# Kernel tuning notes

Hardware: AMD Instinct MI355X
Metric: run time of the kernel (lower is better)

## Reference

```python
import jax, jax.numpy as jnp
import numpy as np

B, H, W, C = 8, 64, 64, 256
RC = C // 8  # reduced channels per build()

def setup_inputs() -> dict:
    key = jax.random.key(0)
    ks = jax.random.split(key, 4)
    x = jax.random.normal(ks[0], (B, H, W, C), dtype=jnp.float32)
    # 1x1 conv kernels flattened to [Cin, Cout]; glorot-ish scale
    wq = jax.random.normal(ks[1], (C, RC), dtype=jnp.float32) * (1.0 / np.sqrt(C))
    wk = jax.random.normal(ks[2], (C, RC), dtype=jnp.float32) * (1.0 / np.sqrt(C))
    wv = jax.random.normal(ks[3], (C, C), dtype=jnp.float32) * (1.0 / np.sqrt(C))
    bq = jnp.zeros((RC,), dtype=jnp.float32)
    bk = jnp.zeros((RC,), dtype=jnp.float32)
    bv = jnp.zeros((C,), dtype=jnp.float32)
    return {"x": x, "wq": wq, "bq": bq, "wk": wk, "bk": bk, "wv": wv, "bv": bv}

def reference(x, wq, bq, wk, bk, wv, bv):
    b, h, w, c = x.shape
    n = h * w
    # 1x1 convs == per-pixel channel matmuls; q/k have relu activation, v does not
    q = jax.nn.relu(jnp.einsum('bhwc,cd->bhwd', x, wq) + bq).reshape(b, n, -1)  # [B,N,RC]
    k = jax.nn.relu(jnp.einsum('bhwc,cd->bhwd', x, wk) + bk).reshape(b, n, -1)  # [B,N,RC]
    v = (jnp.einsum('bhwc,cd->bhwd', x, wv) + bv).reshape(b, n, c)              # [B,N,C]
    attn = jax.nn.softmax(jnp.einsum('bnd,bmd->bnm', q, k), axis=-1)            # [B,N,N]
    out = jnp.einsum('bnm,bmc->bnc', attn, v).reshape(b, h, w, c)
    return out + x
```

## Files before the change

kernel.cpp:

```cpp
#include <hip/hip_runtime.h>
#include <hip/hip_bf16.h>

typedef __attribute__((ext_vector_type(8))) short s16x8;
typedef __attribute__((ext_vector_type(4))) float f32x4;
typedef __attribute__((ext_vector_type(4))) unsigned int u32x4;

#define BATCH 8
#define NPIX  4096
#define CCH   256
#define RCH   32
#define TK    32
#define HALFK 2048
#define NIT   (HALFK / TK)
#define THR   8.0f
#define LOG2E 1.4426950408889634f

__device__ __forceinline__ unsigned short f2bf(float f) {
  __hip_bfloat16 h = __float2bfloat16(f);
  return __builtin_bit_cast(unsigned short, h);
}

__device__ __forceinline__ unsigned int cvt_pk(float lo, float hi) {
  unsigned int r;
  asm("v_cvt_pk_bf16_f32 %0, %1, %2" : "=v"(r) : "v"(lo), "v"(hi));
  return r;
}

__global__ void prep_kernel(const float* __restrict__ x,
                            const float* __restrict__ wq,
                            const float* __restrict__ wk,
                            const float* __restrict__ wv,
                            unsigned short* __restrict__ xb,
                            unsigned short* __restrict__ wqkT,
                            unsigned short* __restrict__ wvT) {
  int stride = gridDim.x * blockDim.x;
  int i0 = blockIdx.x * blockDim.x + threadIdx.x;
  const int nx4 = BATCH * NPIX * CCH / 4;
  for (int i = i0; i < nx4; i += stride) {
    float4 v = reinterpret_cast<const float4*>(x)[i];
    ushort4 o;
    o.x = f2bf(v.x); o.y = f2bf(v.y); o.z = f2bf(v.z); o.w = f2bf(v.w);
    reinterpret_cast<ushort4*>(xb)[i] = o;
  }
  for (int i = i0; i < 64 * CCH; i += stride) {
    int d = i >> 8, c = i & 255;
    float v = (d < RCH) ? wq[c * RCH + d] : wk[c * RCH + (d - RCH)];
    wqkT[i] = f2bf(v);
  }
  for (int i = i0; i < CCH * CCH; i += stride) {
    int d = i >> 8, c = i & 255;
    wvT[i] = f2bf(wv[c * CCH + d]);
  }
}

__global__ void proj_kernel(const unsigned short* __restrict__ xb,
                            const unsigned short* __restrict__ wqkT,
                            const unsigned short* __restrict__ wvT,
                            const float* __restrict__ bq,
                            const float* __restrict__ bk,
                            const float* __restrict__ bv,
                            unsigned short* __restrict__ qb,
                            unsigned short* __restrict__ kb,
                            unsigned short* __restrict__ vT) {
  int t = threadIdx.x;
  int w = t >> 6, l = t & 63, g = l >> 4, lc = l & 15;
  f32x4 zero = {0.f, 0.f, 0.f, 0.f};

  if (blockIdx.x < 512) {
    int row0 = blockIdx.x * 64 + w * 16;
    f32x4 acc[4];
    for (int ct = 0; ct < 4; ++ct) acc[ct] = zero;
    for (int ks = 0; ks < 8; ++ks) {
      s16x8 a = *reinterpret_cast<const s16x8*>(
          xb + (size_t)(row0 + lc) * CCH + ks * 32 + g * 8);
      for (int ct = 0; ct < 4; ++ct) {
        s16x8 bfr = *reinterpret_cast<const s16x8*>(
            wqkT + (size_t)(ct * 16 + lc) * CCH + ks * 32 + g * 8);
        acc[ct] = __builtin_amdgcn_mfma_f32_16x16x32_bf16(a, bfr, acc[ct], 0, 0, 0);
      }
    }
    for (int ct = 0; ct < 4; ++ct) {
      int col = ct * 16 + lc;
      float bias = (col < RCH) ? bq[col] : bk[col - RCH];
      for (int r = 0; r < 4; ++r) {
        int row = row0 + 4 * g + r;
        float v = fmaxf(acc[ct][r] + bias, 0.f);
        if (col < RCH) qb[(size_t)row * RCH + col] = f2bf(v * LOG2E);
        else           kb[(size_t)row * RCH + (col - RCH)] = f2bf(v);
      }
    }
  } else {
    int idx = blockIdx.x - 512;
    int b = idx & 7; idx >>= 3;
    int dt = idx & 3; int nt = idx >> 2;
    int d0 = dt * 64 + w * 16;
    int n0 = nt * 64;
    f32x4 acc[4];
    for (int ct = 0; ct < 4; ++ct) acc[ct] = zero;
    for (int ks = 0; ks < 8; ++ks) {
      s16x8 a = *reinterpret_cast<const s16x8*>(
          wvT + (size_t)(d0 + lc) * CCH + ks * 32 + g * 8);
      for (int ct = 0; ct < 4; ++ct) {
        s16x8 bfr = *reinterpret_cast<const s16x8*>(
            xb + ((size_t)b * NPIX + n0 + ct * 16 + lc) * CCH + ks * 32 + g * 8);
        acc[ct] = __builtin_amdgcn_mfma_f32_16x16x32_bf16(a, bfr, acc[ct], 0, 0, 0);
      }
    }
    for (int ct = 0; ct < 4; ++ct) {
      for (int r = 0; r < 4; ++r) {
        int d = d0 + 4 * g + r;
        int n = n0 + ct * 16 + lc;
        vT[((size_t)b * CCH + d) * NPIX + n] = f2bf(acc[ct][r] + bv[d]);
      }
    }
  }
}

__global__ __launch_bounds__(256, 2)
void attn_kernel(const unsigned short* __restrict__ qb,
                 const unsigned short* __restrict__ kb,
                 const unsigned short* __restrict__ vT,
                 const float* __restrict__ x,
                 float* __restrict__ out) {
  __shared__ __attribute__((aligned(16))) unsigned short Vlds[2][CCH * 64];
  __shared__ __attribute__((aligned(16))) float mergeLS[2][32];
  __shared__ float mLds[2];

  int b  = blockIdx.x & 7;
  int qt = blockIdx.x >> 3;
  int t  = threadIdx.x;
  int w = t >> 6, l = t & 63, g = l >> 4, lc = l & 15;
  int a = w >> 1, s = w & 1;
  const size_t bN = (size_t)b * NPIX;
  f32x4 zero = {0.f, 0.f, 0.f, 0.f};

  const unsigned short* kbase = kb + bN * RCH;
  const unsigned short* vbase = vT + (size_t)b * CCH * NPIX;

  int qbase = qt * 64 + a * 32;
  s16x8 qfA = *reinterpret_cast<const s16x8*>(qb + (bN + qbase + lc) * RCH + g * 8);
  s16x8 qfB = *reinterpret_cast<const s16x8*>(qb + (bN + qbase + 16 + lc) * RCH + g * 8);

  int chb = t >> 3, gr = t & 7;
  int gsw = gr ^ (chb & 7);
  int koff = (gsw < 4) ? (gsw * 8) : (HALFK + (gsw - 4) * 8);
  const unsigned short* vsrc = vbase + (size_t)chb * NPIX + koff;

  int krb = 8 * (lc >> 2) + (lc & 3);
  int kO  = s * HALFK + krb;

  unsigned int swz = (lc & 7) << 4;
  int vrS = (s * 64 + g * 16) ^ swz;

  s16x8 ones;
  #pragma unroll
  for (int i = 0; i < 8; ++i) ones[i] = (short)0x3F80;

  f32x4 o[2][16];
  #pragma unroll
  for (int qh = 0; qh < 2; ++qh)
    #pragma unroll
    for (int cc = 0; cc < 16; ++cc) o[qh][cc] = zero;
  f32x4 ols[2];
  ols[0] = zero; ols[1] = zero;
  float m = 0.f;
  f32x4 mneg = zero;

  s16x8 gv[8];
  #pragma unroll
  for (int i = 0; i < 8; ++i)
    gv[i] = *reinterpret_cast<const s16x8*>(vsrc + (size_t)i * 32 * NPIX);
  s16x8 kf0 = *reinterpret_cast<const s16x8*>(kbase + (size_t)(kO + 0) * RCH + g * 8);
  s16x8 kf1 = *reinterpret_cast<const s16x8*>(kbase + (size_t)(kO + 4) * RCH + g * 8);
  #pragma unroll
  for (int i = 0; i < 8; ++i)
    *reinterpret_cast<s16x8*>((char*)&Vlds[0][0] + i * 4096 + t * 16) = gv[i];

  for (int it = 0; it < NIT; ++it) {
    int p = it & 1;
    int kv = it * TK;
    bool nx = (it + 1) < NIT;

    if (nx) {
      #pragma unroll
      for (int i = 0; i < 8; ++i)
        gv[i] = *reinterpret_cast<const s16x8*>(
            vsrc + kv + TK + (size_t)i * 32 * NPIX);
    }

    f32x4 sA0 = __builtin_amdgcn_mfma_f32_16x16x32_bf16(kf0, qfA, mneg, 0, 0, 0);
    f32x4 sA1 = __builtin_amdgcn_mfma_f32_16x16x32_bf16(kf1, qfA, mneg, 0, 0, 0);
    f32x4 sB0 = __builtin_amdgcn_mfma_f32_16x16x32_bf16(kf0, qfB, mneg, 0, 0, 0);
    f32x4 sB1 = __builtin_amdgcn_mfma_f32_16x16x32_bf16(kf1, qfB, mneg, 0, 0, 0);

    if (nx) {
      kf0 = *reinterpret_cast<const s16x8*>(
          kbase + (size_t)(kO + kv + TK + 0) * RCH + g * 8);
      kf1 = *reinterpret_cast<const s16x8*>(
          kbase + (size_t)(kO + kv + TK + 4) * RCH + g * 8);
    }

    float xA = fmaxf(fmaxf(sA0[0], sA0[1]), fmaxf(sA0[2], sA0[3]));
    float xB = fmaxf(fmaxf(sA1[0], sA1[1]), fmaxf(sA1[2], sA1[3]));
    float xC = fmaxf(fmaxf(sB0[0], sB0[1]), fmaxf(sB0[2], sB0[3]));
    float xD = fmaxf(fmaxf(sB1[0], sB1[1]), fmaxf(sB1[2], sB1[3]));
    float pmax = fmaxf(fmaxf(xA, xB), fmaxf(xC, xD));

    float sc = 1.f;
    int resc = !__all(pmax <= THR);
    if (resc) {
      #pragma unroll
      for (int off = 1; off <= 32; off <<= 1)
        pmax = fmaxf(pmax, __shfl_xor(pmax, off));
      float delta = fmaxf(pmax, 0.f);
      sc = exp2f(-delta);
      m += delta;
      f32x4 dd = {delta, delta, delta, delta};
      mneg -= dd;
      sA0 -= dd; sA1 -= dd; sB0 -= dd; sB1 -= dd;
      #pragma unroll
      for (int qh = 0; qh < 2; ++qh) {
        #pragma unroll
        for (int cc = 0; cc < 16; ++cc)
          #pragma unroll
          for (int r = 0; r < 4; ++r) o[qh][cc][r] *= sc;
        #pragma unroll
        for (int r = 0; r < 4; ++r) ols[qh][r] *= sc;
      }
    }

    unsigned int pkA[4], pkB[4];
    pkA[0] = cvt_pk(exp2f(sA0[0]), exp2f(sA0[1]));
    pkA[1] = cvt_pk(exp2f(sA0[2]), exp2f(sA0[3]));
    pkA[2] = cvt_pk(exp2f(sA1[0]), exp2f(sA1[1]));
    pkA[3] = cvt_pk(exp2f(sA1[2]), exp2f(sA1[3]));
    pkB[0] = cvt_pk(exp2f(sB0[0]), exp2f(sB0[1]));
    pkB[1] = cvt_pk(exp2f(sB0[2]), exp2f(sB0[3]));
    pkB[2] = cvt_pk(exp2f(sB1[0]), exp2f(sB1[1]));
    pkB[3] = cvt_pk(exp2f(sB1[2]), exp2f(sB1[3]));

    u32x4 uA = {pkA[0], pkA[1], pkA[2], pkA[3]};
    u32x4 uB = {pkB[0], pkB[1], pkB[2], pkB[3]};
    s16x8 paA = __builtin_bit_cast(s16x8, uA);
    s16x8 paB = __builtin_bit_cast(s16x8, uB);
    ols[0] = __builtin_amdgcn_mfma_f32_16x16x32_bf16(paA, ones, ols[0], 0, 0, 0);
    ols[1] = __builtin_amdgcn_mfma_f32_16x16x32_bf16(paB, ones, ols[1], 0, 0, 0);

    asm volatile("s_waitcnt lgkmcnt(0)" ::: "memory");
    __builtin_amdgcn_s_barrier();
    asm volatile("" ::: "memory");

    const char* pb = (const char*)&Vlds[p][0] + lc * 128 + vrS;
    __builtin_amdgcn_s_setprio(1);
    #pragma unroll
    for (int cc = 0; cc < 16; ++cc) {
      s16x8 vb = *reinterpret_cast<const s16x8*>(pb + cc * 2048);
      o[0][cc] = __builtin_amdgcn_mfma_f32_16x16x32_bf16(paA, vb, o[0][cc], 0, 0, 0);
      o[1][cc] = __builtin_amdgcn_mfma_f32_16x16x32_bf16(paB, vb, o[1][cc], 0, 0, 0);
    }
    __builtin_amdgcn_s_setprio(0);

    if (nx) {
      #pragma unroll
      for (int i = 0; i < 8; ++i)
        *reinterpret_cast<s16x8*>((char*)&Vlds[p ^ 1][0] + i * 4096 + t * 16) = gv[i];
    }
  }

  if (s == 1) {
    if (lc == 0) {
      *reinterpret_cast<f32x4*>(&mergeLS[a][4 * g])      = ols[0];
      *reinterpret_cast<f32x4*>(&mergeLS[a][16 + 4 * g]) = ols[1];
    }
    if (l == 0) mLds[a] = m;
  }
  __syncthreads();

  float* mrg = (float*)&Vlds[0][0];
  if (s == 1) {
    float* base = mrg + a * 8192 + l * 128;
    #pragma unroll
    for (int qh = 0; qh < 2; ++qh)
      #pragma unroll
      for (int cc = 0; cc < 16; ++cc) {
        int idx = qh * 16 + cc;
        *reinterpret_cast<f32x4*>(base + ((idx + l) & 31) * 4) = o[qh][cc];
      }
  }
  __syncthreads();
  if (s == 0) {
    float mB = mLds[a];
    float mT = fmaxf(m, mB);
    float sAc = exp2f(m - mT), sBc = exp2f(mB - mT);
    const float* base = mrg + a * 8192 + l * 128;
    #pragma unroll
    for (int qh = 0; qh < 2; ++qh) {
      f32x4 lB4 = *reinterpret_cast<const f32x4*>(&mergeLS[a][qh * 16 + 4 * g]);
      f32x4 rl;
      #pragma unroll
      for (int r = 0; r < 4; ++r)
        rl[r] = 1.0f / (ols[qh][r] * sAc + lB4[r] * sBc);
      #pragma unroll
      for (int cc = 0; cc < 16; ++cc) {
        int idx = qh * 16 + cc;
        f32x4 ob = *reinterpret_cast<const f32x4*>(base + ((idx + l) & 31) * 4);
        #pragma unroll
        for (int r = 0; r < 4; ++r) {
          size_t row = bN + qbase + qh * 16 + 4 * g + r;
          size_t oi = row * CCH + cc * 16 + lc;
          out[oi] = (o[qh][cc][r] * sAc + ob[r] * sBc) * rl[r] + x[oi];
        }
      }
    }
  }
}

extern "C" void kernel_launch(void* const* d_in, const int* in_sizes, int n_in,
                              void* d_out, int out_size, void* d_ws, size_t ws_size,
                              hipStream_t stream) {
  const float* x  = (const float*)d_in[0];
  const float* wq = (const float*)d_in[1];
  const float* bq = (const float*)d_in[2];
  const float* wk = (const float*)d_in[3];
  const float* bk = (const float*)d_in[4];
  const float* wv = (const float*)d_in[5];
  const float* bv = (const float*)d_in[6];
  float* out = (float*)d_out;

  unsigned short* ws   = (unsigned short*)d_ws;
  unsigned short* qb   = ws;
  unsigned short* kb   = qb + 1048576;
  unsigned short* vT   = kb + 1048576;
  unsigned short* xb   = vT + 8388608;
  unsigned short* wqkT = xb + 8388608;
  unsigned short* wvT  = wqkT + 16384;

  prep_kernel<<<dim3(2048), dim3(256), 0, stream>>>(x, wq, wk, wv, xb, wqkT, wvT);
  proj_kernel<<<dim3(2560), dim3(256), 0, stream>>>(xb, wqkT, wvT, bq, bk, bv,
                                                    qb, kb, vT);
  attn_kernel<<<dim3(512), dim3(256), 0, stream>>>(qb, kb, vT, x, out);
}
```

Baseline: 166.6 us.

## Software-pipeline QK softmax one tile ahead and stream V via direct global-to-LDS loads

Replaces register-staged V loads and LDS stores with global_load_lds direct copies into the double buffer. Restructures the loop so the QK scores and exp for the next tile are computed after the current PV MFMAs, overlapping softmax VALU work with matrix work. The rescale still happens before the next P is formed, but the barrier moves to the end of the iteration. It risks wait-count and synchronisation subtleties around the direct-to-LDS loads and adds register pressure from carrying P across iterations.

```diff
diff --git a/kernel.cpp b/kernel.cpp
--- a/kernel.cpp
+++ b/kernel.cpp
@@ -24,6 +24,12 @@
   unsigned int r;
   asm("v_cvt_pk_bf16_f32 %0, %1, %2" : "=v"(r) : "v"(lo), "v"(hi));
   return r;
+}
+
+__device__ __forceinline__ void gload_lds16(const void* g, void* l) {
+  __builtin_amdgcn_global_load_lds(
+      (const __attribute__((address_space(1))) void*)g,
+      (__attribute__((address_space(3))) void*)l, 16, 0, 0);
 }
 
 __global__ void prep_kernel(const float* __restrict__ x,
@@ -166,90 +172,78 @@
   float m = 0.f;
   f32x4 mneg = zero;
 
-  s16x8 gv[8];
   #pragma unroll
   for (int i = 0; i < 8; ++i)
-    gv[i] = *reinterpret_cast<const s16x8*>(vsrc + (size_t)i * 32 * NPIX);
-  s16x8 kf0 = *reinterpret_cast<const s16x8*>(kbase + (size_t)(kO + 0) * RCH + g * 8);
-  s16x8 kf1 = *reinterpret_cast<const s16x8*>(kbase + (size_t)(kO + 4) * RCH + g * 8);
-  #pragma unroll
-  for (int i = 0; i < 8; ++i)
-    *reinterpret_cast<s16x8*>((char*)&Vlds[0][0] + i * 4096 + t * 16) = gv[i];
-
-  for (int it = 0; it < NIT; ++it) {
-    int p = it & 1;
-    int kv = it * TK;
-    bool nx = (it + 1) < NIT;
-
-    if (nx) {
-      #pragma unroll
-      for (int i = 0; i < 8; ++i)
-        gv[i] = *reinterpret_cast<const s16x8*>(
-            vsrc + kv + TK + (size_t)i * 32 * NPIX);
-    }
-
-    f32x4 sA0 = __builtin_amdgcn_mfma_f32_16x16x32_bf16(kf0, qfA, mneg, 0, 0, 0);
-    f32x4 sA1 = __builtin_amdgcn_mfma_f32_16x16x32_bf16(kf1, qfA, mneg, 0, 0, 0);
-    f32x4 sB0 = __builtin_amdgcn_mfma_f32_16x16x32_bf16(kf0, qfB, mneg, 0, 0, 0);
-    f32x4 sB1 = __builtin_amdgcn_mfma_f32_16x16x32_bf16(kf1, qfB, mneg, 0, 0, 0);
-
-    if (nx) {
-      kf0 = *reinterpret_cast<const s16x8*>(
-          kbase + (size_t)(kO + kv + TK + 0) * RCH + g * 8);
-      kf1 = *reinterpret_cast<const s16x8*>(
-          kbase + (size_t)(kO + kv + TK + 4) * RCH + g * 8);
-    }
+    gload_lds16(vsrc + (size_t)i * 32 * NPIX,
+                (char*)&Vlds[0][0] + i * 4096 + t * 16);
+  s16x8 paA, paB;
+  s16x8 kf0, kf1;
+  {
+    s16x8 ka = *reinterpret_cast<const s16x8*>(kbase + (size_t)(kO + 0) * RCH + g * 8);
+    s16x8 kb2 = *reinterpret_cast<const s16x8*>(kbase + (size_t)(kO + 4) * RCH + g * 8);
+    f32x4 sA0 = __builtin_amdgcn_mfma_f32_16x16x32_bf16(ka, qfA, zero, 0, 0, 0);
+    f32x4 sA1 = __builtin_amdgcn_mfma_f32_16x16x32_bf16(kb2, qfA, zero, 0, 0, 0);
+    f32x4 sB0 = __builtin_amdgcn_mfma_f32_16x16x32_bf16(ka, qfB, zero, 0, 0, 0);
+    f32x4 sB1 = __builtin_amdgcn_mfma_f32_16x16x32_bf16(kb2, qfB, zero, 0, 0, 0);
+    kf0 = *reinterpret_cast<const s16x8*>(kbase + (size_t)(kO + TK + 0) * RCH + g * 8);
+    kf1 = *reinterpret_cast<const s16x8*>(kbase + (size_t)(kO + TK + 4) * RCH + g * 8);
 
     float xA = fmaxf(fmaxf(sA0[0], sA0[1]), fmaxf(sA0[2], sA0[3]));
     float xB = fmaxf(fmaxf(sA1[0], sA1[1]), fmaxf(sA1[2], sA1[3]));
     float xC = fmaxf(fmaxf(sB0[0], sB0[1]), fmaxf(sB0[2], sB0[3]));
     float xD = fmaxf(fmaxf(sB1[0], sB1[1]), fmaxf(sB1[2], sB1[3]));
     float pmax = fmaxf(fmaxf(xA, xB), fmaxf(xC, xD));
-
-    float sc = 1.f;
     int resc = !__all(pmax <= THR);
     if (resc) {
       #pragma unroll
       for (int off = 1; off <= 32; off <<= 1)
         pmax = fmaxf(pmax, __shfl_xor(pmax, off));
       float delta = fmaxf(pmax, 0.f);
-      sc = exp2f(-delta);
       m += delta;
       f32x4 dd = {delta, delta, delta, delta};
       mneg -= dd;
       sA0 -= dd; sA1 -= dd; sB0 -= dd; sB1 -= dd;
-      #pragma unroll
-      for (int qh = 0; qh < 2; ++qh) {
-        #pragma unroll
-        for (int cc = 0; cc < 16; ++cc)
-          #pragma unroll
-          for (int r = 0; r < 4; ++r) o[qh][cc][r] *= sc;
-        #pragma unroll
-        for (int r = 0; r < 4; ++r) ols[qh][r] *= sc;
-      }
-    }
-
-    unsigned int pkA[4], pkB[4];
-    pkA[0] = cvt_pk(exp2f(sA0[0]), exp2f(sA0[1]));
-    pkA[1] = cvt_pk(exp2f(sA0[2]), exp2f(sA0[3]));
-    pkA[2] = cvt_pk(exp2f(sA1[0]), exp2f(sA1[1]));
-    pkA[3] = cvt_pk(exp2f(sA1[2]), exp2f(sA1[3]));
-    pkB[0] = cvt_pk(exp2f(sB0[0]), exp2f(sB0[1]));
-    pkB[1] = cvt_pk(exp2f(sB0[2]), exp2f(sB0[3]));
-    pkB[2] = cvt_pk(exp2f(sB1[0]), exp2f(sB1[1]));
-    pkB[3] = cvt_pk(exp2f(sB1[2]), exp2f(sB1[3]));
-
-    u32x4 uA = {pkA[0], pkA[1], pkA[2], pkA[3]};
-    u32x4 uB = {pkB[0], pkB[1], pkB[2], pkB[3]};
-    s16x8 paA = __builtin_bit_cast(s16x8, uA);
-    s16x8 paB = __builtin_bit_cast(s16x8, uB);
+    }
+    u32x4 uA = {cvt_pk(exp2f(sA0[0]), exp2f(sA0[1])),
+                cvt_pk(exp2f(sA0[2]), exp2f(sA0[3])),
+                cvt_pk(exp2f(sA1[0]), exp2f(sA1[1])),
+                cvt_pk(exp2f(sA1[2]), exp2f(sA1[3]))};
+    u32x4 uB = {cvt_pk(exp2f(sB0[0]), exp2f(sB0[1])),
+                cvt_pk(exp2f(sB0[2]), exp2f(sB0[3])),
+                cvt_pk(exp2f(sB1[0]), exp2f(sB1[1])),
+                cvt_pk(exp2f(sB1[2]), exp2f(sB1[3]))};
+    paA = __builtin_bit_cast(s16x8, uA);
+    paB = __builtin_bit_cast(s16x8, uB);
+  }
+  __syncthreads();
+
+  for (int it = 0; it < NIT; ++it) {
+    int p = it & 1;
+    bool nx = (it + 1) < NIT;
+    int kvn = (it + 1) * TK;
+
+    if (nx) {
+      #pragma unroll
+      for (int i = 0; i < 8; ++i)
+        gload_lds16(vsrc + kvn + (size_t)i * 32 * NPIX,
+                    (char*)&Vlds[p ^ 1][0] + i * 4096 + t * 16);
+    }
+
+    f32x4 sA0, sA1, sB0, sB1;
+    if (nx) {
+      sA0 = __builtin_amdgcn_mfma_f32_16x16x32_bf16(kf0, qfA, mneg, 0, 0, 0);
+      sA1 = __builtin_amdgcn_mfma_f32_16x16x32_bf16(kf1, qfA, mneg, 0, 0, 0);
+      sB0 = __builtin_amdgcn_mfma_f32_16x16x32_bf16(kf0, qfB, mneg, 0, 0, 0);
+      sB1 = __builtin_amdgcn_mfma_f32_16x16x32_bf16(kf1, qfB, mneg, 0, 0, 0);
+      int kv2 = (kvn + TK) & (HALFK - 1);
+      kf0 = *reinterpret_cast<const s16x8*>(
+          kbase + (size_t)(kO + kv2 + 0) * RCH + g * 8);
+      kf1 = *reinterpret_cast<const s16x8*>(
+          kbase + (size_t)(kO + kv2 + 4) * RCH + g * 8);
+    }
+
     ols[0] = __builtin_amdgcn_mfma_f32_16x16x32_bf16(paA, ones, ols[0], 0, 0, 0);
     ols[1] = __builtin_amdgcn_mfma_f32_16x16x32_bf16(paB, ones, ols[1], 0, 0, 0);
-
-    asm volatile("s_waitcnt lgkmcnt(0)" ::: "memory");
-    __builtin_amdgcn_s_barrier();
-    asm volatile("" ::: "memory");
-
     const char* pb = (const char*)&Vlds[p][0] + lc * 128 + vrS;
     __builtin_amdgcn_s_setprio(1);
     #pragma unroll
@@ -261,9 +255,43 @@
     __builtin_amdgcn_s_setprio(0);
 
     if (nx) {
-      #pragma unroll
-      for (int i = 0; i < 8; ++i)
-        *reinterpret_cast<s16x8*>((char*)&Vlds[p ^ 1][0] + i * 4096 + t * 16) = gv[i];
+      float xA = fmaxf(fmaxf(sA0[0], sA0[1]), fmaxf(sA0[2], sA0[3]));
+      float xB = fmaxf(fmaxf(sA1[0], sA1[1]), fmaxf(sA1[2], sA1[3]));
+      float xC = fmaxf(fmaxf(sB0[0], sB0[1]), fmaxf(sB0[2], sB0[3]));
+      float xD = fmaxf(fmaxf(sB1[0], sB1[1]), fmaxf(sB1[2], sB1[3]));
+      float pmax = fmaxf(fmaxf(xA, xB), fmaxf(xC, xD));
+      int resc = !__all(pmax <= THR);
+      if (resc) {
+        #pragma unroll
+        for (int off = 1; off <= 32; off <<= 1)
+          pmax = fmaxf(pmax, __shfl_xor(pmax, off));
+        float delta = fmaxf(pmax, 0.f);
+        float sc = exp2f(-delta);
+        m += delta;
+        f32x4 dd = {delta, delta, delta, delta};
+        mneg -= dd;
+        sA0 -= dd; sA1 -= dd; sB0 -= dd; sB1 -= dd;
+        #pragma unroll
+        for (int qh = 0; qh < 2; ++qh) {
+          #pragma unroll
+          for (int cc = 0; cc < 16; ++cc)
+            #pragma unroll
+            for (int r = 0; r < 4; ++r) o[qh][cc][r] *= sc;
+          #pragma unroll
+          for (int r = 0; r < 4; ++r) ols[qh][r] *= sc;
+        }
+      }
+      u32x4 uA = {cvt_pk(exp2f(sA0[0]), exp2f(sA0[1])),
+                  cvt_pk(exp2f(sA0[2]), exp2f(sA0[3])),
+                  cvt_pk(exp2f(sA1[0]), exp2f(sA1[1])),
+                  cvt_pk(exp2f(sA1[2]), exp2f(sA1[3]))};
+      u32x4 uB = {cvt_pk(exp2f(sB0[0]), exp2f(sB0[1])),
+                  cvt_pk(exp2f(sB0[2]), exp2f(sB0[3])),
+                  cvt_pk(exp2f(sB1[0]), exp2f(sB1[1])),
+                  cvt_pk(exp2f(sB1[2]), exp2f(sB1[3]))};
+      paA = __builtin_bit_cast(s16x8, uA);
+      paB = __builtin_bit_cast(s16x8, uB);
+      __syncthreads();
     }
   }
 
```

Measured after the change: 172.7 us. 1.04x slower.
